# Kernel tuning notes

Measured on AMD Instinct MI355X. Metric: run time of the kernel, lower is better.

## Reference

```python
import jax, jax.numpy as jnp
import numpy as np
from jax import lax

EPS = 1e-5      # BatchNorm eps
SLOPE = 0.01    # LeakyReLU negative slope
SHIFT = 0.5     # ShiftedLeakyReLU downward shift (assumed)

# sign with clipped straight-through estimator (hardtanh STE)
@jax.custom_vjp
def binarize(x):
    return jnp.sign(x)

def _bin_fwd(x):
    return jnp.sign(x), x

def _bin_bwd(res, g):
    x = res
    return (g * (jnp.abs(x) <= 1.0).astype(g.dtype),)

binarize.defvjp(_bin_fwd, _bin_bwd)


def conv2d(x, w, b, stride, padding, groups):
    # x: [B,Cin,H,W], w: [Cout,Cin//groups,kh,kw]
    y = lax.conv_general_dilated(
        x, w,
        window_strides=(stride, stride),
        padding=[(padding, padding), (padding, padding)],
        dimension_numbers=('NCHW', 'OIHW', 'NCHW'),
        feature_group_count=groups,
    )
    return y + b[None, :, None, None]


def batchnorm(x, gamma, beta):
    # training-mode BN: batch statistics over (N,H,W)
    mean = jnp.mean(x, axis=(0, 2, 3), keepdims=True)
    var = jnp.var(x, axis=(0, 2, 3), keepdims=True)
    xn = (x - mean) * lax.rsqrt(var + EPS)
    return xn * gamma[None, :, None, None] + beta[None, :, None, None]


def shifted_leaky_relu(x):
    return jax.nn.leaky_relu(x, SLOPE) - SHIFT


def block(x, w, b, gamma, beta, stride, padding, groups, binarize_w):
    wq = binarize(w) if binarize_w else w
    x = conv2d(x, wq, b, stride, padding, groups)
    x = batchnorm(x, gamma, beta)
    x = shifted_leaky_relu(x)
    return binarize(x)


def setup_inputs() -> dict:
    D, B, C, NCLS = 10000, 16, 1, 10
    key = jax.random.key(0)
    ks = jax.random.split(key, 6)
    u = lambda k, shape: jax.random.uniform(k, shape, jnp.float32, -1.0, 1.0)
    return {
        "x":  jax.random.normal(ks[0], (B, C, 28, 28), jnp.float32),
        "W1": u(ks[1], (D, C, 5, 5)),  "b1": jnp.zeros((D,), jnp.float32),
        "g1": jnp.ones((D,), jnp.float32), "be1": jnp.zeros((D,), jnp.float32),
        "W2": u(ks[2], (D, 1, 3, 3)),  "b2": jnp.zeros((D,), jnp.float32),
        "g2": jnp.ones((D,), jnp.float32), "be2": jnp.zeros((D,), jnp.float32),
        "W3": u(ks[3], (D, 1, 6, 6)) * 0.1, "b3": jnp.zeros((D,), jnp.float32),
        "g3": jnp.ones((D,), jnp.float32), "be3": jnp.zeros((D,), jnp.float32),
        "Wc": u(ks[4], (NCLS, D)),
    }


def reference(x, W1, b1, g1, be1, W2, b2, g2, be2, W3, b3, g3, be3, Wc):
    D = Wc.shape[1]
    # encoder: binary conv -> BN -> shifted leaky relu -> binarize
    h = block(x, W1, b1, g1, be1, stride=2, padding=1, groups=1, binarize_w=True)   # [B,D,13,13]
    h = block(h, W2, b2, g2, be2, stride=2, padding=0, groups=D, binarize_w=True)   # [B,D,6,6]
    # final prototype conv (plain fp32 weights, depthwise, collapses spatial dims)
    h = block(h, W3, b3, g3, be3, stride=1, padding=0, groups=D, binarize_w=False)  # [B,D,1,1]
    h = h.reshape(h.shape[0], -1)                                                   # [B,D]
    # centroid similarity with sign-binarized class hypervectors
    sims = h @ binarize(Wc).T                                                       # [B,n_classes]
    return sims / jnp.sqrt(jnp.float32(D))
```

## Files before the change

### kernel.cpp

```cpp
#include <hip/hip_runtime.h>
#include <stdint.h>

__device__ __forceinline__ float sgnf(float v) {
    return (v > 0.f) ? 1.f : ((v < 0.f) ? -1.f : 0.f);
}

__global__ void prep_w1(const float* __restrict__ W1, float* __restrict__ w1q) {
    const int i = blockIdx.x * 256 + threadIdx.x;
    if (i < 250000) w1q[i] = sgnf(W1[i]);
}

__global__ __launch_bounds__(256, 2) void hdc_fused(
    const float* __restrict__ x,  const float* __restrict__ w1q,
    const float* __restrict__ b1, const float* __restrict__ g1,
    const float* __restrict__ be1,
    const float* __restrict__ W2, const float* __restrict__ b2,
    const float* __restrict__ g2, const float* __restrict__ be2,
    const float* __restrict__ W3, const float* __restrict__ b3,
    const float* __restrict__ g3, const float* __restrict__ be3,
    const float* __restrict__ Wc, const float* __restrict__ zrow,
    float* __restrict__ out)
{
    __shared__ signed char h1s[8 * 2704];
    __shared__ float redbuf[4][4];
    __shared__ float h3buf[8 * 16];

    const int tid  = threadIdx.x;
    const int base = blockIdx.x * 8;

    const bool act = (tid < 208);
    const int oy = tid >> 4, bb = tid & 15;
    const int wv = tid >> 6, ln = tid & 63;

    for (int sg = 0; sg < 4; ++sg) {
        const int d0 = base + 2 * sg, d1 = d0 + 1;

        const float* __restrict__ wpa = w1q + d0 * 25;
        float wa[25], wb[25];
        #pragma unroll
        for (int k = 0; k < 25; ++k) { wa[k] = wpa[k]; wb[k] = wpa[25 + k]; }

        const float b1a = b1[d0], b1b = b1[d1];
        float fa[13], fb[13];
        #pragma unroll
        for (int i = 0; i < 13; ++i) { fa[i] = b1a; fb[i] = b1b; }

        if (act) {
            #pragma unroll
            for (int ky = 0; ky < 5; ++ky) {
                const int rr_ = 2 * oy - 1 + ky;
                const float* rp = (rr_ >= 0) ? (x + bb * 784 + rr_ * 28) : zrow;
                float r[29];
                r[0] = 0.f;
                #pragma unroll
                for (int j = 0; j < 7; ++j) {
                    float4 v = ((const float4*)rp)[j];
                    r[4 * j + 1] = v.x; r[4 * j + 2] = v.y;
                    r[4 * j + 3] = v.z; r[4 * j + 4] = v.w;
                }
                #pragma unroll
                for (int kx = 0; kx < 5; ++kx) {
                    const float wka = wa[5 * ky + kx], wkb = wb[5 * ky + kx];
                    #pragma unroll
                    for (int ox = 0; ox < 13; ++ox) {
                        const float xv = r[2 * ox + kx];
                        fa[ox] = fmaf(xv, wka, fa[ox]);
                        fb[ox] = fmaf(xv, wkb, fb[ox]);
                    }
                }
            }
        }

        float sa = 0.f, sb = 0.f;
        if (act) {
            #pragma unroll
            for (int i = 0; i < 13; ++i) { sa += fa[i]; sb += fb[i]; }
        }
        #pragma unroll
        for (int m = 32; m >= 1; m >>= 1) {
            sa += __shfl_xor(sa, m, 64);
            sb += __shfl_xor(sb, m, 64);
        }
        if (ln == 0) { redbuf[wv][0] = sa; redbuf[wv][1] = sb; }
        __syncthreads();
        const float mua = (redbuf[0][0] + redbuf[1][0] + redbuf[2][0] + redbuf[3][0]) / 2704.f;
        const float mub = (redbuf[0][1] + redbuf[1][1] + redbuf[2][1] + redbuf[3][1]) / 2704.f;

        float da = 0.f, db = 0.f;
        if (act) {
            #pragma unroll
            for (int i = 0; i < 13; ++i) {
                const float ea = fa[i] - mua, eb = fb[i] - mub;
                da = fmaf(ea, ea, da);
                db = fmaf(eb, eb, db);
            }
        }
        #pragma unroll
        for (int m = 32; m >= 1; m >>= 1) {
            da += __shfl_xor(da, m, 64);
            db += __shfl_xor(db, m, 64);
        }
        if (ln == 0) { redbuf[wv][2] = da; redbuf[wv][3] = db; }
        __syncthreads();
        const float iva = rsqrtf((redbuf[0][2] + redbuf[1][2] + redbuf[2][2] + redbuf[3][2]) / 2704.f + 1e-5f);
        const float ivb = rsqrtf((redbuf[0][3] + redbuf[1][3] + redbuf[2][3] + redbuf[3][3]) / 2704.f + 1e-5f);

        if (act) {
            const float ga = g1[d0], gb = g1[d1];
            const float bea = be1[d0], beb = be1[d1];
            signed char* ha = &h1s[(2 * sg) * 2704 + bb * 169 + oy * 13];
            signed char* hb = &h1s[(2 * sg + 1) * 2704 + bb * 169 + oy * 13];
            #pragma unroll
            for (int i = 0; i < 13; ++i) {
                const float xna = (fa[i] - mua) * iva;
                const float ya  = fmaf(xna, ga, bea);
                const float za  = ((ya > 0.f) ? ya : 0.01f * ya) - 0.5f;
                ha[i] = (za > 0.f) ? 1 : ((za < 0.f) ? -1 : 0);
                const float xnb = (fb[i] - mub) * ivb;
                const float yb  = fmaf(xnb, gb, beb);
                const float zb  = ((yb > 0.f) ? yb : 0.01f * yb) - 0.5f;
                hb[i] = (zb > 0.f) ? 1 : ((zb < 0.f) ? -1 : 0);
            }
        }
        __syncthreads();
    }

    if (tid < 128) {
        const int ch = tid >> 4, b_ = tid & 15;
        const int d = base + ch;
        float sw2[9];
        #pragma unroll
        for (int k = 0; k < 9; ++k) sw2[k] = sgnf(W2[d * 9 + k]);
        const float b2v = b2[d];
        const signed char* hp = &h1s[ch * 2704 + b_ * 169];

        float c2[36];
        #pragma unroll
        for (int oy2 = 0; oy2 < 6; ++oy2) {
            float rr[3][13];
            #pragma unroll
            for (int ky = 0; ky < 3; ++ky)
                #pragma unroll
                for (int j = 0; j < 13; ++j)
                    rr[ky][j] = (float)hp[(2 * oy2 + ky) * 13 + j];
            #pragma unroll
            for (int ox2 = 0; ox2 < 6; ++ox2) {
                float s = b2v;
                #pragma unroll
                for (int ky = 0; ky < 3; ++ky)
                    #pragma unroll
                    for (int kx = 0; kx < 3; ++kx)
                        s = fmaf(rr[ky][2 * ox2 + kx], sw2[3 * ky + kx], s);
                c2[oy2 * 6 + ox2] = s;
            }
        }

        float s2 = 0.f;
        #pragma unroll
        for (int i = 0; i < 36; ++i) s2 += c2[i];
        #pragma unroll
        for (int m = 8; m >= 1; m >>= 1) s2 += __shfl_xor(s2, m, 16);
        const float mu2 = s2 / 576.f;
        float d2 = 0.f;
        #pragma unroll
        for (int i = 0; i < 36; ++i) { const float e = c2[i] - mu2; d2 = fmaf(e, e, d2); }
        #pragma unroll
        for (int m = 8; m >= 1; m >>= 1) d2 += __shfl_xor(d2, m, 16);
        const float inv2 = rsqrtf(d2 / 576.f + 1e-5f);
        const float g2v = g2[d], be2v = be2[d];

        float z3 = b3[d];
        #pragma unroll
        for (int i = 0; i < 36; ++i) {
            const float xn = (c2[i] - mu2) * inv2;
            const float y  = fmaf(xn, g2v, be2v);
            const float z  = ((y > 0.f) ? y : 0.01f * y) - 0.5f;
            const float h2 = (z > 0.f) ? 1.f : ((z < 0.f) ? -1.f : 0.f);
            z3 = fmaf(h2, W3[d * 36 + i], z3);
        }

        float s3 = z3;
        #pragma unroll
        for (int m = 8; m >= 1; m >>= 1) s3 += __shfl_xor(s3, m, 16);
        const float mu3 = s3 / 16.f;
        const float e3 = z3 - mu3;
        float d3 = e3 * e3;
        #pragma unroll
        for (int m = 8; m >= 1; m >>= 1) d3 += __shfl_xor(d3, m, 16);
        const float inv3 = rsqrtf(d3 / 16.f + 1e-5f);
        const float xn3 = (z3 - mu3) * inv3;
        const float y3  = fmaf(xn3, g3[d], be3[d]);
        const float zz  = ((y3 > 0.f) ? y3 : 0.01f * y3) - 0.5f;
        h3buf[tid] = (zz > 0.f) ? 1.f : ((zz < 0.f) ? -1.f : 0.f);
    }
    __syncthreads();

    if (tid < 160) {
        const int bq = tid / 10, cq = tid - bq * 10;
        float ssum = 0.f;
        #pragma unroll
        for (int ch = 0; ch < 8; ++ch)
            ssum += h3buf[ch * 16 + bq] * sgnf(Wc[cq * 10000 + base + ch]);
        atomicAdd(&out[bq * 10 + cq], ssum);
    }
}

__global__ void hdc_scale(float* __restrict__ out) {
    const int i = threadIdx.x;
    if (i < 160) out[i] = out[i] / 100.0f;
}

extern "C" void kernel_launch(void* const* d_in, const int* in_sizes, int n_in,
                              void* d_out, int out_size, void* d_ws, size_t ws_size,
                              hipStream_t stream) {
    const float* x   = (const float*)d_in[0];
    const float* W1  = (const float*)d_in[1];
    const float* b1  = (const float*)d_in[2];
    const float* g1  = (const float*)d_in[3];
    const float* be1 = (const float*)d_in[4];
    const float* W2  = (const float*)d_in[5];
    const float* b2  = (const float*)d_in[6];
    const float* g2  = (const float*)d_in[7];
    const float* be2 = (const float*)d_in[8];
    const float* W3  = (const float*)d_in[9];
    const float* b3  = (const float*)d_in[10];
    const float* g3  = (const float*)d_in[11];
    const float* be3 = (const float*)d_in[12];
    const float* Wc  = (const float*)d_in[13];
    float* out  = (float*)d_out;
    float* w1q  = (float*)d_ws;
    float* zrow = (float*)d_ws + 250000;

    hipMemsetAsync(out, 0, 160 * sizeof(float), stream);
    hipMemsetAsync(zrow, 0, 128, stream);

    prep_w1<<<dim3(977), dim3(256), 0, stream>>>(W1, w1q);
    hdc_fused<<<dim3(1250), dim3(256), 0, stream>>>(
        x, w1q, b1, g1, be1, W2, b2, g2, be2, W3, b3, g3, be3, Wc, zrow, out);
    hdc_scale<<<dim3(1), dim3(192), 0, stream>>>(out);
}
```

Baseline: 81.93 us.

## Rebalance channel work per block, cut registers, and fold memsets and scale into kernels

Grid grows from 1250 to 2048 blocks: 904 blocks take 6 channels and the rest take 4, so the load spreads more evenly across CUs. Launch bounds rise to 4 blocks per SM. Register pressure drops by streaming W1 weights from memory instead of holding them in registers, splitting each row window into two halves, and recomputing stage-2 conv values three times instead of keeping a 36-element array. The two memsets and the scale kernel are folded into prep_w1 and the final atomic add, cutting launch overhead. The h1 shared-memory layout is padded for aligned packed byte loads, and the sign of Wc is staged in shared memory.

```diff
diff --git a/kernel.cpp b/kernel.cpp
--- a/kernel.cpp
+++ b/kernel.cpp
@@ -1,16 +1,24 @@
 #include <hip/hip_runtime.h>
 #include <stdint.h>
 
+#define H1B 176
+#define H1C 2816
+
 __device__ __forceinline__ float sgnf(float v) {
     return (v > 0.f) ? 1.f : ((v < 0.f) ? -1.f : 0.f);
 }
 
-__global__ void prep_w1(const float* __restrict__ W1, float* __restrict__ w1q) {
+__global__ void prep_w1(const float* __restrict__ W1, float* __restrict__ w1q,
+                        float* __restrict__ out, float* __restrict__ zrow) {
     const int i = blockIdx.x * 256 + threadIdx.x;
     if (i < 250000) w1q[i] = sgnf(W1[i]);
-}
-
-__global__ __launch_bounds__(256, 2) void hdc_fused(
+    if (blockIdx.x == 0) {
+        if (threadIdx.x < 160) out[threadIdx.x] = 0.f;
+        else if (threadIdx.x < 192) zrow[threadIdx.x - 160] = 0.f;
+    }
+}
+
+__global__ __launch_bounds__(256, 4) void hdc_fused(
     const float* __restrict__ x,  const float* __restrict__ w1q,
     const float* __restrict__ b1, const float* __restrict__ g1,
     const float* __restrict__ be1,
@@ -21,24 +29,24 @@
     const float* __restrict__ Wc, const float* __restrict__ zrow,
     float* __restrict__ out)
 {
-    __shared__ signed char h1s[8 * 2704];
-    __shared__ float redbuf[4][4];
-    __shared__ float h3buf[8 * 16];
-
-    const int tid  = threadIdx.x;
-    const int base = blockIdx.x * 8;
+    __shared__ __align__(16) signed char h1s[6 * H1C];
+    __shared__ float redbuf[3][4][4];
+    __shared__ float h3buf[6 * 16];
+    __shared__ float wcs[60];
+
+    const int tid = threadIdx.x;
+    const bool heavy = (blockIdx.x < 904);
+    const int nch  = heavy ? 6 : 4;
+    const int nsw  = heavy ? 3 : 2;
+    const int base = heavy ? blockIdx.x * 6 : 5424 + (blockIdx.x - 904) * 4;
 
     const bool act = (tid < 208);
     const int oy = tid >> 4, bb = tid & 15;
     const int wv = tid >> 6, ln = tid & 63;
 
-    for (int sg = 0; sg < 4; ++sg) {
+    for (int sg = 0; sg < nsw; ++sg) {
         const int d0 = base + 2 * sg, d1 = d0 + 1;
-
-        const float* __restrict__ wpa = w1q + d0 * 25;
-        float wa[25], wb[25];
-        #pragma unroll
-        for (int k = 0; k < 25; ++k) { wa[k] = wpa[k]; wb[k] = wpa[25 + k]; }
+        const float* __restrict__ wp = w1q + d0 * 25;
 
         const float b1a = b1[d0], b1b = b1[d1];
         float fa[13], fb[13];
@@ -50,22 +58,44 @@
             for (int ky = 0; ky < 5; ++ky) {
                 const int rr_ = 2 * oy - 1 + ky;
                 const float* rp = (rr_ >= 0) ? (x + bb * 784 + rr_ * 28) : zrow;
-                float r[29];
-                r[0] = 0.f;
-                #pragma unroll
-                for (int j = 0; j < 7; ++j) {
-                    float4 v = ((const float4*)rp)[j];
-                    r[4 * j + 1] = v.x; r[4 * j + 2] = v.y;
-                    r[4 * j + 3] = v.z; r[4 * j + 4] = v.w;
+
+                {
+                    float ra[17];
+                    ra[0] = 0.f;
+                    #pragma unroll
+                    for (int j = 0; j < 4; ++j) {
+                        float4 v = ((const float4*)rp)[j];
+                        ra[4 * j + 1] = v.x; ra[4 * j + 2] = v.y;
+                        ra[4 * j + 3] = v.z; ra[4 * j + 4] = v.w;
+                    }
+                    #pragma unroll
+                    for (int kx = 0; kx < 5; ++kx) {
+                        const float wka = wp[5 * ky + kx], wkb = wp[25 + 5 * ky + kx];
+                        #pragma unroll
+                        for (int ox = 0; ox < 7; ++ox) {
+                            const float xv = ra[2 * ox + kx];
+                            fa[ox] = fmaf(xv, wka, fa[ox]);
+                            fb[ox] = fmaf(xv, wkb, fb[ox]);
+                        }
+                    }
                 }
-                #pragma unroll
-                for (int kx = 0; kx < 5; ++kx) {
-                    const float wka = wa[5 * ky + kx], wkb = wb[5 * ky + kx];
-                    #pragma unroll
-                    for (int ox = 0; ox < 13; ++ox) {
-                        const float xv = r[2 * ox + kx];
-                        fa[ox] = fmaf(xv, wka, fa[ox]);
-                        fb[ox] = fmaf(xv, wkb, fb[ox]);
+                {
+                    float rb[16];
+                    #pragma unroll
+                    for (int j = 0; j < 4; ++j) {
+                        float4 v = ((const float4*)rp)[3 + j];
+                        rb[4 * j + 0] = v.x; rb[4 * j + 1] = v.y;
+                        rb[4 * j + 2] = v.z; rb[4 * j + 3] = v.w;
+                    }
+                    #pragma unroll
+                    for (int kx = 0; kx < 5; ++kx) {
+                        const float wka = wp[5 * ky + kx], wkb = wp[25 + 5 * ky + kx];
+                        #pragma unroll
+                        for (int ox = 7; ox < 13; ++ox) {
+                            const float xv = rb[2 * ox + kx - 13];
+                            fa[ox] = fmaf(xv, wka, fa[ox]);
+                            fb[ox] = fmaf(xv, wkb, fb[ox]);
+                        }
                     }
                 }
             }
@@ -81,10 +111,12 @@
             sa += __shfl_xor(sa, m, 64);
             sb += __shfl_xor(sb, m, 64);
         }
-        if (ln == 0) { redbuf[wv][0] = sa; redbuf[wv][1] = sb; }
+        if (ln == 0) { redbuf[sg][wv][0] = sa; redbuf[sg][wv][1] = sb; }
         __syncthreads();
-        const float mua = (redbuf[0][0] + redbuf[1][0] + redbuf[2][0] + redbuf[3][0]) / 2704.f;
-        const float mub = (redbuf[0][1] + redbuf[1][1] + redbuf[2][1] + redbuf[3][1]) / 2704.f;
+        const float mua = (redbuf[sg][0][0] + redbuf[sg][1][0]
+                         + redbuf[sg][2][0] + redbuf[sg][3][0]) / 2704.f;
+        const float mub = (redbuf[sg][0][1] + redbuf[sg][1][1]
+                         + redbuf[sg][2][1] + redbuf[sg][3][1]) / 2704.f;
 
         float da = 0.f, db = 0.f;
         if (act) {
@@ -100,16 +132,18 @@
             da += __shfl_xor(da, m, 64);
             db += __shfl_xor(db, m, 64);
         }
-        if (ln == 0) { redbuf[wv][2] = da; redbuf[wv][3] = db; }
+        if (ln == 0) { redbuf[sg][wv][2] = da; redbuf[sg][wv][3] = db; }
         __syncthreads();
-        const float iva = rsqrtf((redbuf[0][2] + redbuf[1][2] + redbuf[2][2] + redbuf[3][2]) / 2704.f + 1e-5f);
-        const float ivb = rsqrtf((redbuf[0][3] + redbuf[1][3] + redbuf[2][3] + redbuf[3][3]) / 2704.f + 1e-5f);
+        const float iva = rsqrtf((redbuf[sg][0][2] + redbuf[sg][1][2]
+                                + redbuf[sg][2][2] + redbuf[sg][3][2]) / 2704.f + 1e-5f);
+        const float ivb = rsqrtf((redbuf[sg][0][3] + redbuf[sg][1][3]
+                                + redbuf[sg][2][3] + redbuf[sg][3][3]) / 2704.f + 1e-5f);
 
         if (act) {
             const float ga = g1[d0], gb = g1[d1];
             const float bea = be1[d0], beb = be1[d1];
-            signed char* ha = &h1s[(2 * sg) * 2704 + bb * 169 + oy * 13];
-            signed char* hb = &h1s[(2 * sg + 1) * 2704 + bb * 169 + oy * 13];
+            signed char* ha = &h1s[(2 * sg) * H1C + bb * H1B + oy * 13];
+            signed char* hb = &h1s[(2 * sg + 1) * H1C + bb * H1B + oy * 13];
             #pragma unroll
             for (int i = 0; i < 13; ++i) {
                 const float xna = (fa[i] - mua) * iva;
@@ -122,48 +156,67 @@
                 hb[i] = (zb > 0.f) ? 1 : ((zb < 0.f) ? -1 : 0);
             }
         }
-        __syncthreads();
-    }
-
-    if (tid < 128) {
+    }
+    __syncthreads();
+
+#define LOAD_WIN(oy2)                                                         \
+    const int c0 = (26 * (oy2)) & ~15;                                        \
+    uint32_t w[16];                                                           \
+    {   const uint4* p4 = (const uint4*)(hrow + c0);                          \
+        _Pragma("unroll")                                                     \
+        for (int j = 0; j < 4; ++j) {                                         \
+            uint4 v = p4[j];                                                  \
+            w[4 * j + 0] = v.x; w[4 * j + 1] = v.y;                           \
+            w[4 * j + 2] = v.z; w[4 * j + 3] = v.w;                           \
+        }                                                                     \
+    }
+#define C2VAL(oy2, ox2, dst)                                                  \
+    float dst = b2v;                                                          \
+    _Pragma("unroll")                                                         \
+    for (int ky = 0; ky < 3; ++ky) {                                          \
+        _Pragma("unroll")                                                     \
+        for (int kx = 0; kx < 3; ++kx) {                                      \
+            const int ib = (2 * (oy2) + ky) * 13 + 2 * (ox2) + kx - c0;       \
+            dst = fmaf((float)((signed char)(w[ib >> 2] >> ((ib & 3) * 8))),  \
+                       sw2[3 * ky + kx], dst);                                \
+        }                                                                     \
+    }
+
+    if (tid < 16 * nch) {
         const int ch = tid >> 4, b_ = tid & 15;
         const int d = base + ch;
+        const signed char* hrow = &h1s[ch * H1C + b_ * H1B];
+
         float sw2[9];
         #pragma unroll
         for (int k = 0; k < 9; ++k) sw2[k] = sgnf(W2[d * 9 + k]);
         const float b2v = b2[d];
-        const signed char* hp = &h1s[ch * 2704 + b_ * 169];
-
-        float c2[36];
+
+        float s2 = 0.f;
         #pragma unroll
         for (int oy2 = 0; oy2 < 6; ++oy2) {
-            float rr[3][13];
-            #pragma unroll
-            for (int ky = 0; ky < 3; ++ky)
-                #pragma unroll
-                for (int j = 0; j < 13; ++j)
-                    rr[ky][j] = (float)hp[(2 * oy2 + ky) * 13 + j];
+            LOAD_WIN(oy2)
             #pragma unroll
             for (int ox2 = 0; ox2 < 6; ++ox2) {
-                float s = b2v;
-                #pragma unroll
-                for (int ky = 0; ky < 3; ++ky)
-                    #pragma unroll
-                    for (int kx = 0; kx < 3; ++kx)
-                        s = fmaf(rr[ky][2 * ox2 + kx], sw2[3 * ky + kx], s);
-                c2[oy2 * 6 + ox2] = s;
-            }
-        }
-
-        float s2 = 0.f;
-        #pragma unroll
-        for (int i = 0; i < 36; ++i) s2 += c2[i];
+                C2VAL(oy2, ox2, sacc)
+                s2 += sacc;
+            }
+        }
         #pragma unroll
         for (int m = 8; m >= 1; m >>= 1) s2 += __shfl_xor(s2, m, 16);
         const float mu2 = s2 / 576.f;
+
         float d2 = 0.f;
         #pragma unroll
-        for (int i = 0; i < 36; ++i) { const float e = c2[i] - mu2; d2 = fmaf(e, e, d2); }
+        for (int oy2 = 0; oy2 < 6; ++oy2) {
+            LOAD_WIN(oy2)
+            #pragma unroll
+            for (int ox2 = 0; ox2 < 6; ++ox2) {
+                C2VAL(oy2, ox2, sacc)
+                const float e = sacc - mu2;
+                d2 = fmaf(e, e, d2);
+            }
+        }
         #pragma unroll
         for (int m = 8; m >= 1; m >>= 1) d2 += __shfl_xor(d2, m, 16);
         const float inv2 = rsqrtf(d2 / 576.f + 1e-5f);
@@ -171,12 +224,17 @@
 
         float z3 = b3[d];
         #pragma unroll
-        for (int i = 0; i < 36; ++i) {
-            const float xn = (c2[i] - mu2) * inv2;
-            const float y  = fmaf(xn, g2v, be2v);
-            const float z  = ((y > 0.f) ? y : 0.01f * y) - 0.5f;
-            const float h2 = (z > 0.f) ? 1.f : ((z < 0.f) ? -1.f : 0.f);
-            z3 = fmaf(h2, W3[d * 36 + i], z3);
+        for (int oy2 = 0; oy2 < 6; ++oy2) {
+            LOAD_WIN(oy2)
+            #pragma unroll
+            for (int ox2 = 0; ox2 < 6; ++ox2) {
+                C2VAL(oy2, ox2, sacc)
+                const float xn = (sacc - mu2) * inv2;
+                const float y  = fmaf(xn, g2v, be2v);
+                const float z  = ((y > 0.f) ? y : 0.01f * y) - 0.5f;
+                const float h2 = (z > 0.f) ? 1.f : ((z < 0.f) ? -1.f : 0.f);
+                z3 = fmaf(h2, W3[d * 36 + oy2 * 6 + ox2], z3);
+            }
         }
 
         float s3 = z3;
@@ -192,22 +250,21 @@
         const float y3  = fmaf(xn3, g3[d], be3[d]);
         const float zz  = ((y3 > 0.f) ? y3 : 0.01f * y3) - 0.5f;
         h3buf[tid] = (zz > 0.f) ? 1.f : ((zz < 0.f) ? -1.f : 0.f);
-    }
+    } else if (tid >= 192) {
+        for (int i = tid - 192; i < 10 * nch; i += 64)
+            wcs[i] = sgnf(Wc[(i % 10) * 10000 + base + (i / 10)]);
+    }
+#undef LOAD_WIN
+#undef C2VAL
     __syncthreads();
 
     if (tid < 160) {
         const int bq = tid / 10, cq = tid - bq * 10;
         float ssum = 0.f;
-        #pragma unroll
-        for (int ch = 0; ch < 8; ++ch)
-            ssum += h3buf[ch * 16 + bq] * sgnf(Wc[cq * 10000 + base + ch]);
-        atomicAdd(&out[bq * 10 + cq], ssum);
-    }
-}
-
-__global__ void hdc_scale(float* __restrict__ out) {
-    const int i = threadIdx.x;
-    if (i < 160) out[i] = out[i] / 100.0f;
+        for (int ch = 0; ch < nch; ++ch)
+            ssum += h3buf[ch * 16 + bq] * wcs[ch * 10 + cq];
+        atomicAdd(&out[bq * 10 + cq], ssum / 100.0f);
+    }
 }
 
 extern "C" void kernel_launch(void* const* d_in, const int* in_sizes, int n_in,
@@ -231,11 +288,7 @@
     float* w1q  = (float*)d_ws;
     float* zrow = (float*)d_ws + 250000;
 
-    hipMemsetAsync(out, 0, 160 * sizeof(float), stream);
-    hipMemsetAsync(zrow, 0, 128, stream);
-
-    prep_w1<<<dim3(977), dim3(256), 0, stream>>>(W1, w1q);
-    hdc_fused<<<dim3(1250), dim3(256), 0, stream>>>(
+    prep_w1<<<dim3(977), dim3(256), 0, stream>>>(W1, w1q, out, zrow);
+    hdc_fused<<<dim3(2048), dim3(256), 0, stream>>>(
         x, w1q, b1, g1, be1, W2, b2, g2, be2, W3, b3, g3, be3, Wc, zrow, out);
-    hdc_scale<<<dim3(1), dim3(192), 0, stream>>>(out);
-}
+}
```

Result: slower. 101.3 us (+23.7%).
